# Performance work log

Measured on AMD Instinct MI355X. Metric: run time of the kernel, lower is better.

Reference implementation:

```python
import jax, jax.numpy as jnp
import numpy as np

E = 128      # embed_dim
NH = 4       # num_heads
HD = E // NH # head_dim = 32
ND = 5       # num_domains
LN_EPS = 1e-5


def setup_inputs() -> dict:
    key = jax.random.key(0)
    ks = jax.random.split(key, 16)
    B, C, D, H, W = 4, 128, 32, 64, 64
    s = 0.02
    return {
        "x": jax.random.normal(ks[0], (B, C, D, H, W), dtype=jnp.float32),
        "domain_idx": jax.random.randint(ks[1], (B,), 0, ND),
        "emb": jax.random.normal(ks[2], (ND, E), dtype=jnp.float32) * s,
        "q_proj_w": jax.random.normal(ks[3], (E, E), dtype=jnp.float32) * s,
        "q_proj_b": jnp.zeros((E,), jnp.float32),
        "wq": jax.random.normal(ks[4], (E, E), dtype=jnp.float32) * s,
        "bq": jnp.zeros((E,), jnp.float32),
        "wk": jax.random.normal(ks[5], (E, E), dtype=jnp.float32) * s,
        "bk": jnp.zeros((E,), jnp.float32),
        "wv": jax.random.normal(ks[6], (E, E), dtype=jnp.float32) * s,
        "bv": jnp.zeros((E,), jnp.float32),
        "wo": jax.random.normal(ks[7], (E, E), dtype=jnp.float32) * s,
        "bo": jnp.zeros((E,), jnp.float32),
        "ln_g": jnp.ones((E,), jnp.float32),
        "ln_b": jnp.zeros((E,), jnp.float32),
    }


def reference(x, domain_idx, emb, q_proj_w, q_proj_b, wq, bq, wk, bk, wv, bv,
              wo, bo, ln_g, ln_b):
    B, C, D, H, W = x.shape
    xr = x.reshape(B, C, -1).transpose(0, 2, 1)          # (B, N, C) tokens
    # single query from domain embedding
    de = emb[domain_idx]                                  # (B, E)
    q = de @ q_proj_w.T + q_proj_b                        # nn.Linear
    # MHA projections (torch nn.MultiheadAttention semantics)
    qh = (q @ wq.T + bq).reshape(B, NH, HD)               # (B, NH, HD)
    kh = (xr @ wk.T + bk).reshape(B, -1, NH, HD)          # (B, N, NH, HD)
    vh = (xr @ wv.T + bv).reshape(B, -1, NH, HD)
    scale = 1.0 / jnp.sqrt(jnp.float32(HD))
    scores = jnp.einsum('bhd,bnhd->bhn', qh, kh) * scale  # (B, NH, N)
    attn = jax.nn.softmax(scores, axis=-1)
    ctx = jnp.einsum('bhn,bnhd->bhd', attn, vh).reshape(B, E)
    out = ctx @ wo.T + bo                                 # (B, E) single token
    # LayerNorm of the single attended vector (broadcast over N is identical)
    mu = jnp.mean(out, axis=-1, keepdims=True)
    var = jnp.mean((out - mu) ** 2, axis=-1, keepdims=True)
    ln = (out - mu) * jax.lax.rsqrt(var + LN_EPS) * ln_g + ln_b
    xr = xr + ln[:, None, :]                              # residual broadcast-add
    return xr.transpose(0, 2, 1).reshape(B, C, D, H, W)
```

## Files before the change

### kernel.cpp

```cpp
#include <hip/hip_runtime.h>
#include <math.h>

#define E 128
#define NH 4
#define HD 32
#define LN_EPS 1e-5f
#define CHN 128
#define BLK_PER_B 64
#define PW 129

#define BAR_LGKM()    do { asm volatile("s_waitcnt lgkmcnt(0)" ::: "memory"); __builtin_amdgcn_s_barrier(); } while (0)
#define BAR_VM_LGKM() do { asm volatile("s_waitcnt vmcnt(0) lgkmcnt(0)" ::: "memory"); __builtin_amdgcn_s_barrier(); } while (0)

typedef const __attribute__((address_space(1))) void* gas_p;
typedef __attribute__((address_space(3))) void* las_p;
__device__ __forceinline__ void gload_lds16(const float* g, void* l) {
    __builtin_amdgcn_global_load_lds((gas_p)(const void*)g, (las_p)l, 16, 0, 0);
}

typedef float f32x4 __attribute__((ext_vector_type(4)));

__global__ __launch_bounds__(512)
void k0_prep(const int* __restrict__ didx,
             const float* __restrict__ emb,
             const float* __restrict__ qpw, const float* __restrict__ qpb,
             const float* __restrict__ wq, const float* __restrict__ bq,
             const float* __restrict__ wk,
             float* __restrict__ u_s, int B)
{
    __shared__ float wbuf[E * PW];
    __shared__ float de_sh[4][E];
    __shared__ float q_sh[4][E];
    __shared__ float qh_sh[4][E];
    __shared__ int didx_sh[8];
    const int t = threadIdx.x;
    const int bb = t >> 7, c = t & 127;
    const float scale = 0.17677669529663687f;
    if (t < B) didx_sh[t] = didx[t];
    __syncthreads();
    for (int b0 = 0; b0 < B; b0 += 4) {
        const int b = b0 + bb;
        const bool act = b < B;
        if (act) de_sh[bb][c] = emb[(long)didx_sh[b] * E + c];
        for (int i = t; i < E * E; i += 512) wbuf[(i >> 7) * PW + (i & 127)] = qpw[i];
        __syncthreads();
        if (act) {
            float a = qpb[c];
            for (int j = 0; j < E; ++j) a += wbuf[c * PW + j] * de_sh[bb][j];
            q_sh[bb][c] = a;
        }
        __syncthreads();
        for (int i = t; i < E * E; i += 512) wbuf[(i >> 7) * PW + (i & 127)] = wq[i];
        __syncthreads();
        if (act) {
            float a = bq[c];
            for (int j = 0; j < E; ++j) a += wbuf[c * PW + j] * q_sh[bb][j];
            qh_sh[bb][c] = a;
        }
        __syncthreads();
        for (int i = t; i < E * E; i += 512) wbuf[(i >> 7) * PW + (i & 127)] = wk[i];
        __syncthreads();
        if (act) {
            #pragma unroll
            for (int h = 0; h < NH; ++h) {
                float a = 0.f;
                for (int d = 0; d < HD; ++d)
                    a += qh_sh[bb][h * HD + d] * wbuf[(h * HD + d) * PW + c];
                u_s[((long)b * NH + h) * E + c] = a * scale;
            }
        }
        __syncthreads();
    }
}

__global__ __launch_bounds__(512, 2)
void k13_fused(const float* __restrict__ x,
               const float* __restrict__ u_s,
               float* __restrict__ part_ctx,
               float* __restrict__ part_m,
               float* __restrict__ part_l,
               int N, int nk)
{
    __shared__ float4 tile[2][4096];
    __shared__ __align__(16) float p_sh[NH][CHN];
    __shared__ __align__(16) float red_sh[8][32][20];
    __shared__ float lacc[8][NH];

    const int t = threadIdx.x;
    const int lane = t & 63;
    const int wv = t >> 6;
    const int g = blockIdx.x;
    const int b = g >> 6;
    const int bi = g & 63;
    const long xoff = (long)b * E * N;

    const int q    = t & 31;
    const int cseg = t >> 5;
    const int q2   = t >> 4;
    const int th   = t & 15;
    const int n2   = (q2 << 2) | (th >> 2);
    const int h2   = th & 3;

    float u_reg[8][NH];
    #pragma unroll
    for (int j = 0; j < 8; ++j)
        #pragma unroll
        for (int hh = 0; hh < NH; ++hh)
            u_reg[j][hh] = u_s[((long)b * NH + hh) * E + (cseg << 3) + j];

    float l_loc = 0.f;
    float acc[NH][8];
    #pragma unroll
    for (int hh = 0; hh < NH; ++hh)
        #pragma unroll
        for (int j = 0; j < 8; ++j) acc[hh][j] = 0.f;

    auto STAGE = [&](int kk, int buf) {
        const float* xb = x + xoff + (long)(bi * nk + kk) * CHN;
        float4* tb = &tile[buf][0];
        #pragma unroll
        for (int r = 0; r < 8; ++r) {
            const int sbase = ((r << 3) + wv) << 6;
            const int s = sbase + lane;
            const int c = s >> 5, qg = s & 31;
            gload_lds16(xb + (long)c * N + (qg << 2), (void*)&tb[sbase]);
        }
    };

    STAGE(0, 0);
    BAR_VM_LGKM();
    int cur = 0;

    for (int k = 0; k < nk; ++k) {
        if (k + 1 < nk) STAGE(k + 1, cur ^ 1);
        const float4* lt = &tile[cur][0];

        float4 xc[8];
        float sa[4][NH];
        #pragma unroll
        for (int tok = 0; tok < 4; ++tok)
            #pragma unroll
            for (int hh = 0; hh < NH; ++hh) sa[tok][hh] = 0.f;
        #pragma unroll
        for (int j = 0; j < 8; ++j) {
            float4 xq = lt[(((cseg << 3) + j) << 5) + q];
            xc[j] = xq;
            #pragma unroll
            for (int hh = 0; hh < NH; ++hh) {
                const float uv = u_reg[j][hh];
                sa[0][hh] = fmaf(uv, xq.x, sa[0][hh]);
                sa[1][hh] = fmaf(uv, xq.y, sa[1][hh]);
                sa[2][hh] = fmaf(uv, xq.z, sa[2][hh]);
                sa[3][hh] = fmaf(uv, xq.w, sa[3][hh]);
            }
        }
        #pragma unroll
        for (int tok = 0; tok < 4; ++tok)
            #pragma unroll
            for (int hh = 0; hh < NH; ++hh)
                sa[tok][hh] += __shfl_xor(sa[tok][hh], 32);
        if (lane < 32) {
            *(float4*)&red_sh[wv][q][0]  = make_float4(sa[0][0], sa[0][1], sa[0][2], sa[0][3]);
            *(float4*)&red_sh[wv][q][4]  = make_float4(sa[1][0], sa[1][1], sa[1][2], sa[1][3]);
            *(float4*)&red_sh[wv][q][8]  = make_float4(sa[2][0], sa[2][1], sa[2][2], sa[2][3]);
            *(float4*)&red_sh[wv][q][12] = make_float4(sa[3][0], sa[3][1], sa[3][2], sa[3][3]);
        }
        BAR_LGKM();

        float s = red_sh[0][q2][th] + red_sh[1][q2][th]
                + red_sh[2][q2][th] + red_sh[3][q2][th]
                + red_sh[4][q2][th] + red_sh[5][q2][th]
                + red_sh[6][q2][th] + red_sh[7][q2][th];
        float p = __expf(s);
        l_loc += p;
        p_sh[h2][n2] = p;
        BAR_LGKM();

        float4 pq[NH];
        #pragma unroll
        for (int hh = 0; hh < NH; ++hh) pq[hh] = *(const float4*)&p_sh[hh][q << 2];
        #pragma unroll
        for (int j = 0; j < 8; ++j) {
            const float4 xq = xc[j];
            #pragma unroll
            for (int hh = 0; hh < NH; ++hh) {
                float a = acc[hh][j];
                a = fmaf(pq[hh].x, xq.x, a); a = fmaf(pq[hh].y, xq.y, a);
                a = fmaf(pq[hh].z, xq.z, a); a = fmaf(pq[hh].w, xq.w, a);
                acc[hh][j] = a;
            }
        }

        BAR_VM_LGKM();
        cur ^= 1;
    }

    #pragma unroll
    for (int hh = 0; hh < NH; ++hh) {
        #pragma unroll
        for (int j = 0; j < 8; ++j) {
            float v = acc[hh][j];
            #pragma unroll
            for (int o = 16; o > 0; o >>= 1) v += __shfl_xor(v, o);
            if (q == 0)
                part_ctx[((long)g * NH + hh) * E + (cseg << 3) + j] = v;
        }
    }
    float r = l_loc;
    r += __shfl_xor(r, 4); r += __shfl_xor(r, 8);
    r += __shfl_xor(r, 16); r += __shfl_xor(r, 32);
    if (lane < 4) lacc[wv][lane] = r;
    __syncthreads();
    if (t < NH) {
        float L = 0.f;
        #pragma unroll
        for (int w = 0; w < 8; ++w) L += lacc[w][t];
        part_l[g * NH + t] = L;
        part_m[g * NH + t] = 0.f;
    }
}

__global__ __launch_bounds__(512)
void kC_combine_outln(const float* __restrict__ part_ctx,
                      const float* __restrict__ part_m,
                      const float* __restrict__ part_l,
                      const float* __restrict__ wvw, const float* __restrict__ bv,
                      const float* __restrict__ wo, const float* __restrict__ bo,
                      const float* __restrict__ lng, const float* __restrict__ lnb,
                      float* __restrict__ ln_out)
{
    const int b = blockIdx.x;
    const int t = threadIdx.x;
    const int lane = t & 63, wv = t >> 6;
    __shared__ float ef[BLK_PER_B][NH];
    __shared__ float Msh[NH][4], Lsh[NH][4];
    __shared__ float sctx[NH][E];
    __shared__ float ctxv[E];
    __shared__ float wbuf[E * PW];
    __shared__ float redl[512];

    const int ii = t >> 2, hA = t & 3;
    float pm = 0.f, pl = 0.f;
    if (t < 256) {
        pm = part_m[(b * BLK_PER_B + ii) * NH + hA];
        pl = part_l[(b * BLK_PER_B + ii) * NH + hA];
        float mx = pm;
        mx = fmaxf(mx, __shfl_xor(mx, 4));  mx = fmaxf(mx, __shfl_xor(mx, 8));
        mx = fmaxf(mx, __shfl_xor(mx, 16)); mx = fmaxf(mx, __shfl_xor(mx, 32));
        if (lane < 4) Msh[lane][wv] = mx;
    }
    __syncthreads();
    float M[NH];
    #pragma unroll
    for (int h = 0; h < NH; ++h)
        M[h] = fmaxf(fmaxf(Msh[h][0], Msh[h][1]), fmaxf(Msh[h][2], Msh[h][3]));
    if (t < 256) {
        float e = __expf(pm - M[hA]);
        ef[ii][hA] = e;
        float r = pl * e;
        r += __shfl_xor(r, 4); r += __shfl_xor(r, 8);
        r += __shfl_xor(r, 16); r += __shfl_xor(r, 32);
        if (lane < 4) Lsh[lane][wv] = r;
    }
    __syncthreads();
    float invL[NH];
    #pragma unroll
    for (int h = 0; h < NH; ++h)
        invL[h] = 1.f / (Lsh[h][0] + Lsh[h][1] + Lsh[h][2] + Lsh[h][3]);

    const int hB = t >> 7, cB = t & 127;
    const float* pc = part_ctx + (long)b * BLK_PER_B * NH * E;
    float a0 = 0.f, a1 = 0.f, a2 = 0.f, a3 = 0.f;
    for (int i = 0; i < BLK_PER_B; i += 4) {
        a0 += pc[((i + 0) * NH + hB) * E + cB] * ef[i + 0][hB];
        a1 += pc[((i + 1) * NH + hB) * E + cB] * ef[i + 1][hB];
        a2 += pc[((i + 2) * NH + hB) * E + cB] * ef[i + 2][hB];
        a3 += pc[((i + 3) * NH + hB) * E + cB] * ef[i + 3][hB];
    }
    sctx[hB][cB] = (a0 + a1 + a2 + a3) * invL[hB];
    __syncthreads();

    for (int i = t; i < E * E; i += 512) wbuf[(i >> 7) * PW + (i & 127)] = wvw[i];
    __syncthreads();
    float ov = 0.f;
    if (t < E) {
        const int hC = t >> 5;
        float a = bv[t];
        for (int c = 0; c < E; ++c) a += wbuf[t * PW + c] * sctx[hC][c];
        ctxv[t] = a;
    }
    __syncthreads();
    for (int i = t; i < E * E; i += 512) wbuf[(i >> 7) * PW + (i & 127)] = wo[i];
    __syncthreads();
    if (t < E) {
        float o = bo[t];
        for (int i2 = 0; i2 < E; ++i2) o += wbuf[t * PW + i2] * ctxv[i2];
        ov = o;
    }
    redl[t] = (t < E) ? ov : 0.f;
    __syncthreads();
    for (int st = 64; st > 0; st >>= 1) { if (t < st) redl[t] += redl[t + st]; __syncthreads(); }
    const float mu = redl[0] / E;
    __syncthreads();
    const float d = (t < E) ? (ov - mu) : 0.f;
    redl[t] = d * d;
    __syncthreads();
    for (int st = 64; st > 0; st >>= 1) { if (t < st) redl[t] += redl[t + st]; __syncthreads(); }
    const float var = redl[0] / E;
    if (t < E) ln_out[b * E + t] = d * rsqrtf(var + LN_EPS) * lng[t] + lnb[t];
}

__global__ void k5_resid(const float* __restrict__ x, const float* __restrict__ ln,
                         float* __restrict__ out, int sh2, long total4)
{
    long i = (long)blockIdx.x * blockDim.x + threadIdx.x;
    const long stride = (long)gridDim.x * blockDim.x;
    for (; i < total4; i += stride) {
        const int bc = (int)(i >> sh2);
        const float l = ln[bc];
        f32x4 v = ((const f32x4*)x)[i];
        v += l;
        __builtin_nontemporal_store(v, ((f32x4*)out) + i);
    }
}

extern "C" void kernel_launch(void* const* d_in, const int* in_sizes, int n_in,
                              void* d_out, int out_size, void* d_ws, size_t ws_size,
                              hipStream_t stream) {
    const float* x   = (const float*)d_in[0];
    const int*   didx= (const int*)d_in[1];
    const float* emb = (const float*)d_in[2];
    const float* qpw = (const float*)d_in[3];
    const float* qpb = (const float*)d_in[4];
    const float* wq  = (const float*)d_in[5];
    const float* bq  = (const float*)d_in[6];
    const float* wk  = (const float*)d_in[7];
    const float* wvw = (const float*)d_in[9];
    const float* bv  = (const float*)d_in[10];
    const float* wo  = (const float*)d_in[11];
    const float* bo  = (const float*)d_in[12];
    const float* lng = (const float*)d_in[13];
    const float* lnb = (const float*)d_in[14];
    float* out = (float*)d_out;

    const int B = in_sizes[1];
    const long totalx = (long)in_sizes[0];
    const int N = (int)(totalx / ((long)B * E));
    const int nk = N / (CHN * BLK_PER_B);
    int lgN = 0; while ((1 << lgN) < N) ++lgN;
    const int sh2 = lgN - 2;

    float* ws       = (float*)d_ws;
    float* u_s      = ws;
    float* part_m   = u_s      + (long)B * NH * E;
    float* part_l   = part_m   + (long)B * BLK_PER_B * NH;
    float* part_ctx = part_l   + (long)B * BLK_PER_B * NH;
    float* ln_o     = part_ctx + (long)B * BLK_PER_B * NH * E;

    k0_prep<<<1, 512, 0, stream>>>(didx, emb, qpw, qpb, wq, bq, wk, u_s, B);

    k13_fused<<<B * BLK_PER_B, 512, 0, stream>>>(x, u_s, part_ctx, part_m, part_l, N, nk);

    kC_combine_outln<<<B, 512, 0, stream>>>(part_ctx, part_m, part_l,
                                            wvw, bv, wo, bo, lng, lnb, ln_o);

    long total4 = (long)B * E * N / 4;
    k5_resid<<<2048, 256, 0, stream>>>(x, ln_o, out, sh2, total4);
}
```

Before: 162.9 us.

## Fuse attention, output projection, layernorm and residual into one persistent kernel

Replaces the attention-partial, combine and residual kernels with a single persistent kernel of 256 blocks. The blocks loop over batches, accumulate context and softmax denominators with global atomics, and synchronise through a spin-wait grid barrier on a counter. After each barrier every block redundantly computes the V and output projections plus the layernorm, then applies its share of the residual add while prefetching the next batch's tile. This removes launch gaps and the intermediate partial buffers, and lets batch b's residual pass overlap batch b+1's staging. In exchange it adds grid-barrier spin cost, atomic contention, redundant per-block GEMV work, and a deadlock risk if all 256 blocks are not co-resident.

```diff
diff --git a/kernel.cpp b/kernel.cpp
--- a/kernel.cpp
+++ b/kernel.cpp
@@ -6,7 +6,7 @@
 #define HD 32
 #define LN_EPS 1e-5f
 #define CHN 128
-#define BLK_PER_B 64
+#define NBLK 256
 #define PW 129
 
 #define BAR_LGKM()    do { asm volatile("s_waitcnt lgkmcnt(0)" ::: "memory"); __builtin_amdgcn_s_barrier(); } while (0)
@@ -74,25 +74,30 @@
 }
 
 __global__ __launch_bounds__(512, 2)
-void k13_fused(const float* __restrict__ x,
-               const float* __restrict__ u_s,
-               float* __restrict__ part_ctx,
-               float* __restrict__ part_m,
-               float* __restrict__ part_l,
-               int N, int nk)
+void mega(const float* __restrict__ x, const float* __restrict__ u_s,
+          const float* __restrict__ wvw, const float* __restrict__ bv,
+          const float* __restrict__ wo, const float* __restrict__ bo,
+          const float* __restrict__ lng, const float* __restrict__ lnb,
+          float* __restrict__ out,
+          float* __restrict__ ctx_num, float* __restrict__ Lsum,
+          int* __restrict__ cnt,
+          int N, int B, int nk)
 {
     __shared__ float4 tile[2][4096];
     __shared__ __align__(16) float p_sh[NH][CHN];
     __shared__ __align__(16) float red_sh[8][32][20];
     __shared__ float lacc[8][NH];
+    __shared__ float invl_sh[NH];
+    __shared__ __align__(16) float sctx_sh[512];
+    __shared__ float partred[4][128];
+    __shared__ float vec1_sh[128];
+    __shared__ float lnv_sh[128];
+    __shared__ float red512[512];
 
     const int t = threadIdx.x;
     const int lane = t & 63;
-    const int wv = t >> 6;
+    const int wvid = t >> 6;
     const int g = blockIdx.x;
-    const int b = g >> 6;
-    const int bi = g & 63;
-    const long xoff = (long)b * E * N;
 
     const int q    = t & 31;
     const int cseg = t >> 5;
@@ -101,226 +106,193 @@
     const int n2   = (q2 << 2) | (th >> 2);
     const int h2   = th & 3;
 
-    float u_reg[8][NH];
-    #pragma unroll
-    for (int j = 0; j < 8; ++j)
-        #pragma unroll
-        for (int hh = 0; hh < NH; ++hh)
-            u_reg[j][hh] = u_s[((long)b * NH + hh) * E + (cseg << 3) + j];
-
-    float l_loc = 0.f;
-    float acc[NH][8];
-    #pragma unroll
-    for (int hh = 0; hh < NH; ++hh)
-        #pragma unroll
-        for (int j = 0; j < 8; ++j) acc[hh][j] = 0.f;
-
-    auto STAGE = [&](int kk, int buf) {
-        const float* xb = x + xoff + (long)(bi * nk + kk) * CHN;
+    auto STAGE = [&](int bb, int kk, int buf) {
+        const float* xb = x + (long)bb * E * N + (long)(g * nk + kk) * CHN;
         float4* tb = &tile[buf][0];
         #pragma unroll
         for (int r = 0; r < 8; ++r) {
-            const int sbase = ((r << 3) + wv) << 6;
+            const int sbase = ((r << 3) + wvid) << 6;
             const int s = sbase + lane;
             const int c = s >> 5, qg = s & 31;
             gload_lds16(xb + (long)c * N + (qg << 2), (void*)&tb[sbase]);
         }
     };
 
-    STAGE(0, 0);
-    BAR_VM_LGKM();
-    int cur = 0;
-
-    for (int k = 0; k < nk; ++k) {
-        if (k + 1 < nk) STAGE(k + 1, cur ^ 1);
-        const float4* lt = &tile[cur][0];
-
-        float4 xc[8];
-        float sa[4][NH];
+    int epoch = 0;
+    STAGE(0, 0, 0);
+
+    for (int b = 0; b < B; ++b) {
+        float u_reg[8][NH];
         #pragma unroll
-        for (int tok = 0; tok < 4; ++tok)
-            #pragma unroll
-            for (int hh = 0; hh < NH; ++hh) sa[tok][hh] = 0.f;
+        for (int j = 0; j < 8; ++j)
+            #pragma unroll
+            for (int hh = 0; hh < NH; ++hh)
+                u_reg[j][hh] = u_s[((long)b * NH + hh) * E + (cseg << 3) + j];
+
+        float l_loc = 0.f;
+        float acc[NH][8];
         #pragma unroll
-        for (int j = 0; j < 8; ++j) {
-            float4 xq = lt[(((cseg << 3) + j) << 5) + q];
-            xc[j] = xq;
-            #pragma unroll
-            for (int hh = 0; hh < NH; ++hh) {
-                const float uv = u_reg[j][hh];
-                sa[0][hh] = fmaf(uv, xq.x, sa[0][hh]);
-                sa[1][hh] = fmaf(uv, xq.y, sa[1][hh]);
-                sa[2][hh] = fmaf(uv, xq.z, sa[2][hh]);
-                sa[3][hh] = fmaf(uv, xq.w, sa[3][hh]);
-            }
-        }
+        for (int hh = 0; hh < NH; ++hh)
+            #pragma unroll
+            for (int j = 0; j < 8; ++j) acc[hh][j] = 0.f;
+
+        BAR_VM_LGKM();
+        int cur = 0;
+
+        for (int k = 0; k < nk; ++k) {
+            if (k + 1 < nk) STAGE(b, k + 1, cur ^ 1);
+            const float4* lt = &tile[cur][0];
+
+            float4 xc[8];
+            float sa[4][NH];
+            #pragma unroll
+            for (int tok = 0; tok < 4; ++tok)
+                #pragma unroll
+                for (int hh = 0; hh < NH; ++hh) sa[tok][hh] = 0.f;
+            #pragma unroll
+            for (int j = 0; j < 8; ++j) {
+                float4 xq = lt[(((cseg << 3) + j) << 5) + q];
+                xc[j] = xq;
+                #pragma unroll
+                for (int hh = 0; hh < NH; ++hh) {
+                    const float uv = u_reg[j][hh];
+                    sa[0][hh] = fmaf(uv, xq.x, sa[0][hh]);
+                    sa[1][hh] = fmaf(uv, xq.y, sa[1][hh]);
+                    sa[2][hh] = fmaf(uv, xq.z, sa[2][hh]);
+                    sa[3][hh] = fmaf(uv, xq.w, sa[3][hh]);
+                }
+            }
+            #pragma unroll
+            for (int tok = 0; tok < 4; ++tok)
+                #pragma unroll
+                for (int hh = 0; hh < NH; ++hh)
+                    sa[tok][hh] += __shfl_xor(sa[tok][hh], 32);
+            if (lane < 32) {
+                *(float4*)&red_sh[wvid][q][0]  = make_float4(sa[0][0], sa[0][1], sa[0][2], sa[0][3]);
+                *(float4*)&red_sh[wvid][q][4]  = make_float4(sa[1][0], sa[1][1], sa[1][2], sa[1][3]);
+                *(float4*)&red_sh[wvid][q][8]  = make_float4(sa[2][0], sa[2][1], sa[2][2], sa[2][3]);
+                *(float4*)&red_sh[wvid][q][12] = make_float4(sa[3][0], sa[3][1], sa[3][2], sa[3][3]);
+            }
+            BAR_LGKM();
+
+            float s = red_sh[0][q2][th] + red_sh[1][q2][th]
+                    + red_sh[2][q2][th] + red_sh[3][q2][th]
+                    + red_sh[4][q2][th] + red_sh[5][q2][th]
+                    + red_sh[6][q2][th] + red_sh[7][q2][th];
+            float p = __expf(s);
+            l_loc += p;
+            p_sh[h2][n2] = p;
+            BAR_LGKM();
+
+            float4 pq[NH];
+            #pragma unroll
+            for (int hh = 0; hh < NH; ++hh) pq[hh] = *(const float4*)&p_sh[hh][q << 2];
+            #pragma unroll
+            for (int j = 0; j < 8; ++j) {
+                const float4 xq = xc[j];
+                #pragma unroll
+                for (int hh = 0; hh < NH; ++hh) {
+                    float a = acc[hh][j];
+                    a = fmaf(pq[hh].x, xq.x, a); a = fmaf(pq[hh].y, xq.y, a);
+                    a = fmaf(pq[hh].z, xq.z, a); a = fmaf(pq[hh].w, xq.w, a);
+                    acc[hh][j] = a;
+                }
+            }
+            BAR_VM_LGKM();
+            cur ^= 1;
+        }
+
         #pragma unroll
-        for (int tok = 0; tok < 4; ++tok)
-            #pragma unroll
-            for (int hh = 0; hh < NH; ++hh)
-                sa[tok][hh] += __shfl_xor(sa[tok][hh], 32);
-        if (lane < 32) {
-            *(float4*)&red_sh[wv][q][0]  = make_float4(sa[0][0], sa[0][1], sa[0][2], sa[0][3]);
-            *(float4*)&red_sh[wv][q][4]  = make_float4(sa[1][0], sa[1][1], sa[1][2], sa[1][3]);
-            *(float4*)&red_sh[wv][q][8]  = make_float4(sa[2][0], sa[2][1], sa[2][2], sa[2][3]);
-            *(float4*)&red_sh[wv][q][12] = make_float4(sa[3][0], sa[3][1], sa[3][2], sa[3][3]);
-        }
-        BAR_LGKM();
-
-        float s = red_sh[0][q2][th] + red_sh[1][q2][th]
-                + red_sh[2][q2][th] + red_sh[3][q2][th]
-                + red_sh[4][q2][th] + red_sh[5][q2][th]
-                + red_sh[6][q2][th] + red_sh[7][q2][th];
-        float p = __expf(s);
-        l_loc += p;
-        p_sh[h2][n2] = p;
-        BAR_LGKM();
-
-        float4 pq[NH];
-        #pragma unroll
-        for (int hh = 0; hh < NH; ++hh) pq[hh] = *(const float4*)&p_sh[hh][q << 2];
-        #pragma unroll
-        for (int j = 0; j < 8; ++j) {
-            const float4 xq = xc[j];
-            #pragma unroll
-            for (int hh = 0; hh < NH; ++hh) {
-                float a = acc[hh][j];
-                a = fmaf(pq[hh].x, xq.x, a); a = fmaf(pq[hh].y, xq.y, a);
-                a = fmaf(pq[hh].z, xq.z, a); a = fmaf(pq[hh].w, xq.w, a);
-                acc[hh][j] = a;
-            }
-        }
-
-        BAR_VM_LGKM();
-        cur ^= 1;
-    }
-
-    #pragma unroll
-    for (int hh = 0; hh < NH; ++hh) {
-        #pragma unroll
-        for (int j = 0; j < 8; ++j) {
-            float v = acc[hh][j];
-            #pragma unroll
-            for (int o = 16; o > 0; o >>= 1) v += __shfl_xor(v, o);
-            if (q == 0)
-                part_ctx[((long)g * NH + hh) * E + (cseg << 3) + j] = v;
-        }
-    }
-    float r = l_loc;
-    r += __shfl_xor(r, 4); r += __shfl_xor(r, 8);
-    r += __shfl_xor(r, 16); r += __shfl_xor(r, 32);
-    if (lane < 4) lacc[wv][lane] = r;
-    __syncthreads();
-    if (t < NH) {
-        float L = 0.f;
-        #pragma unroll
-        for (int w = 0; w < 8; ++w) L += lacc[w][t];
-        part_l[g * NH + t] = L;
-        part_m[g * NH + t] = 0.f;
-    }
-}
-
-__global__ __launch_bounds__(512)
-void kC_combine_outln(const float* __restrict__ part_ctx,
-                      const float* __restrict__ part_m,
-                      const float* __restrict__ part_l,
-                      const float* __restrict__ wvw, const float* __restrict__ bv,
-                      const float* __restrict__ wo, const float* __restrict__ bo,
-                      const float* __restrict__ lng, const float* __restrict__ lnb,
-                      float* __restrict__ ln_out)
-{
-    const int b = blockIdx.x;
-    const int t = threadIdx.x;
-    const int lane = t & 63, wv = t >> 6;
-    __shared__ float ef[BLK_PER_B][NH];
-    __shared__ float Msh[NH][4], Lsh[NH][4];
-    __shared__ float sctx[NH][E];
-    __shared__ float ctxv[E];
-    __shared__ float wbuf[E * PW];
-    __shared__ float redl[512];
-
-    const int ii = t >> 2, hA = t & 3;
-    float pm = 0.f, pl = 0.f;
-    if (t < 256) {
-        pm = part_m[(b * BLK_PER_B + ii) * NH + hA];
-        pl = part_l[(b * BLK_PER_B + ii) * NH + hA];
-        float mx = pm;
-        mx = fmaxf(mx, __shfl_xor(mx, 4));  mx = fmaxf(mx, __shfl_xor(mx, 8));
-        mx = fmaxf(mx, __shfl_xor(mx, 16)); mx = fmaxf(mx, __shfl_xor(mx, 32));
-        if (lane < 4) Msh[lane][wv] = mx;
-    }
-    __syncthreads();
-    float M[NH];
-    #pragma unroll
-    for (int h = 0; h < NH; ++h)
-        M[h] = fmaxf(fmaxf(Msh[h][0], Msh[h][1]), fmaxf(Msh[h][2], Msh[h][3]));
-    if (t < 256) {
-        float e = __expf(pm - M[hA]);
-        ef[ii][hA] = e;
-        float r = pl * e;
+        for (int hh = 0; hh < NH; ++hh) {
+            #pragma unroll
+            for (int j = 0; j < 8; ++j) {
+                float v = acc[hh][j];
+                #pragma unroll
+                for (int o = 16; o > 0; o >>= 1) v += __shfl_xor(v, o);
+                if (q == 0)
+                    atomicAdd(&ctx_num[((long)b * NH + hh) * E + (cseg << 3) + j], v);
+            }
+        }
+        float r = l_loc;
         r += __shfl_xor(r, 4); r += __shfl_xor(r, 8);
         r += __shfl_xor(r, 16); r += __shfl_xor(r, 32);
-        if (lane < 4) Lsh[lane][wv] = r;
-    }
-    __syncthreads();
-    float invL[NH];
-    #pragma unroll
-    for (int h = 0; h < NH; ++h)
-        invL[h] = 1.f / (Lsh[h][0] + Lsh[h][1] + Lsh[h][2] + Lsh[h][3]);
-
-    const int hB = t >> 7, cB = t & 127;
-    const float* pc = part_ctx + (long)b * BLK_PER_B * NH * E;
-    float a0 = 0.f, a1 = 0.f, a2 = 0.f, a3 = 0.f;
-    for (int i = 0; i < BLK_PER_B; i += 4) {
-        a0 += pc[((i + 0) * NH + hB) * E + cB] * ef[i + 0][hB];
-        a1 += pc[((i + 1) * NH + hB) * E + cB] * ef[i + 1][hB];
-        a2 += pc[((i + 2) * NH + hB) * E + cB] * ef[i + 2][hB];
-        a3 += pc[((i + 3) * NH + hB) * E + cB] * ef[i + 3][hB];
-    }
-    sctx[hB][cB] = (a0 + a1 + a2 + a3) * invL[hB];
-    __syncthreads();
-
-    for (int i = t; i < E * E; i += 512) wbuf[(i >> 7) * PW + (i & 127)] = wvw[i];
-    __syncthreads();
-    float ov = 0.f;
-    if (t < E) {
-        const int hC = t >> 5;
-        float a = bv[t];
-        for (int c = 0; c < E; ++c) a += wbuf[t * PW + c] * sctx[hC][c];
-        ctxv[t] = a;
-    }
-    __syncthreads();
-    for (int i = t; i < E * E; i += 512) wbuf[(i >> 7) * PW + (i & 127)] = wo[i];
-    __syncthreads();
-    if (t < E) {
-        float o = bo[t];
-        for (int i2 = 0; i2 < E; ++i2) o += wbuf[t * PW + i2] * ctxv[i2];
-        ov = o;
-    }
-    redl[t] = (t < E) ? ov : 0.f;
-    __syncthreads();
-    for (int st = 64; st > 0; st >>= 1) { if (t < st) redl[t] += redl[t + st]; __syncthreads(); }
-    const float mu = redl[0] / E;
-    __syncthreads();
-    const float d = (t < E) ? (ov - mu) : 0.f;
-    redl[t] = d * d;
-    __syncthreads();
-    for (int st = 64; st > 0; st >>= 1) { if (t < st) redl[t] += redl[t + st]; __syncthreads(); }
-    const float var = redl[0] / E;
-    if (t < E) ln_out[b * E + t] = d * rsqrtf(var + LN_EPS) * lng[t] + lnb[t];
-}
-
-__global__ void k5_resid(const float* __restrict__ x, const float* __restrict__ ln,
-                         float* __restrict__ out, int sh2, long total4)
-{
-    long i = (long)blockIdx.x * blockDim.x + threadIdx.x;
-    const long stride = (long)gridDim.x * blockDim.x;
-    for (; i < total4; i += stride) {
-        const int bc = (int)(i >> sh2);
-        const float l = ln[bc];
-        f32x4 v = ((const f32x4*)x)[i];
-        v += l;
-        __builtin_nontemporal_store(v, ((f32x4*)out) + i);
+        if (lane < 4) lacc[wvid][lane] = r;
+        __syncthreads();
+        if (t < NH) {
+            float L = 0.f;
+            #pragma unroll
+            for (int w = 0; w < 8; ++w) L += lacc[w][t];
+            atomicAdd(&Lsum[b * NH + t], L);
+        }
+
+        __syncthreads();
+        if (t == 0) {
+            __threadfence();
+            __hip_atomic_fetch_add(cnt, 1, __ATOMIC_ACQ_REL, __HIP_MEMORY_SCOPE_AGENT);
+            const int target = NBLK * (epoch + 1);
+            while (__hip_atomic_load(cnt, __ATOMIC_ACQUIRE, __HIP_MEMORY_SCOPE_AGENT) < target)
+                __builtin_amdgcn_s_sleep(2);
+            __threadfence();
+        }
+        __syncthreads();
+        ++epoch;
+
+        if (t < NH)
+            invl_sh[t] = 1.f / __hip_atomic_load(&Lsum[b * NH + t], __ATOMIC_RELAXED,
+                                                 __HIP_MEMORY_SCOPE_AGENT);
+        __syncthreads();
+        sctx_sh[t] = __hip_atomic_load(&ctx_num[(long)b * NH * E + t], __ATOMIC_RELAXED,
+                                       __HIP_MEMORY_SCOPE_AGENT) * invl_sh[t >> 7];
+        __syncthreads();
+        {
+            const int rr = t & 127, qt = t >> 7;
+            const int hR = rr >> 5;
+            float pa = 0.f;
+            const float* wrow = wvw + rr * E + qt * 32;
+            const float* srow = &sctx_sh[hR * 128 + qt * 32];
+            #pragma unroll
+            for (int c2 = 0; c2 < 32; ++c2) pa = fmaf(wrow[c2], srow[c2], pa);
+            partred[qt][rr] = pa;
+            __syncthreads();
+            if (t < 128)
+                vec1_sh[t] = bv[t] + partred[0][t] + partred[1][t] + partred[2][t] + partred[3][t];
+            __syncthreads();
+            float po = 0.f;
+            const float* worow = wo + rr * E + qt * 32;
+            #pragma unroll
+            for (int c2 = 0; c2 < 32; ++c2) po = fmaf(worow[c2], vec1_sh[qt * 32 + c2], po);
+            partred[qt][rr] = po;
+            __syncthreads();
+            float ov = 0.f;
+            if (t < 128) ov = bo[t] + partred[0][t] + partred[1][t] + partred[2][t] + partred[3][t];
+            red512[t] = (t < 128) ? ov : 0.f;
+            __syncthreads();
+            for (int st = 64; st > 0; st >>= 1) { if (t < st) red512[t] += red512[t + st]; __syncthreads(); }
+            const float mu = red512[0] * (1.f / E);
+            __syncthreads();
+            const float d = (t < 128) ? (ov - mu) : 0.f;
+            red512[t] = d * d;
+            __syncthreads();
+            for (int st = 64; st > 0; st >>= 1) { if (t < st) red512[t] += red512[t + st]; __syncthreads(); }
+            const float var = red512[0] * (1.f / E);
+            if (t < 128) lnv_sh[t] = d * rsqrtf(var + LN_EPS) * lng[t] + lnb[t];
+            __syncthreads();
+        }
+
+        if (b + 1 < B) STAGE(b + 1, 0, 0);
+
+        {
+            const float lnv = lnv_sh[g >> 1];
+            const long base4 = ((long)b * E * N + (long)(g >> 1) * N + (long)(g & 1) * (N >> 1)) >> 2;
+            const f32x4* x4 = (const f32x4*)x;
+            f32x4* o4 = (f32x4*)out;
+            const int seg4 = (N >> 1) >> 2;
+            for (int i = t; i < seg4; i += 512) {
+                f32x4 v = x4[base4 + i];
+                v += lnv;
+                __builtin_nontemporal_store(v, o4 + base4 + i);
+            }
+        }
     }
 }
 
@@ -346,24 +318,18 @@
     const int B = in_sizes[1];
     const long totalx = (long)in_sizes[0];
     const int N = (int)(totalx / ((long)B * E));
-    const int nk = N / (CHN * BLK_PER_B);
-    int lgN = 0; while ((1 << lgN) < N) ++lgN;
-    const int sh2 = lgN - 2;
-
-    float* ws       = (float*)d_ws;
-    float* u_s      = ws;
-    float* part_m   = u_s      + (long)B * NH * E;
-    float* part_l   = part_m   + (long)B * BLK_PER_B * NH;
-    float* part_ctx = part_l   + (long)B * BLK_PER_B * NH;
-    float* ln_o     = part_ctx + (long)B * BLK_PER_B * NH * E;
+    const int nk = N / (CHN * NBLK);
+
+    char* wsb = (char*)d_ws;
+    int*   cnt     = (int*)wsb;
+    float* Lsum    = (float*)(wsb + 128);
+    float* ctx_num = (float*)(wsb + 1024);
+    float* u_s     = (float*)(wsb + 1024 + (long)B * NH * E * 4);
+
+    hipMemsetAsync(d_ws, 0, 1024 + (long)B * NH * E * 4, stream);
 
     k0_prep<<<1, 512, 0, stream>>>(didx, emb, qpw, qpb, wq, bq, wk, u_s, B);
 
-    k13_fused<<<B * BLK_PER_B, 512, 0, stream>>>(x, u_s, part_ctx, part_m, part_l, N, nk);
-
-    kC_combine_outln<<<B, 512, 0, stream>>>(part_ctx, part_m, part_l,
-                                            wvw, bv, wo, bo, lng, lnb, ln_o);
-
-    long total4 = (long)B * E * N / 4;
-    k5_resid<<<2048, 256, 0, stream>>>(x, ln_o, out, sh2, total4);
+    mega<<<NBLK, 512, 0, stream>>>(x, u_s, wvw, bv, wo, bo, lng, lnb, out,
+                                   ctx_num, Lsum, cnt, N, B, nk);
 }
```

After: 453.4 us. 178% more time.
